# Kernel tuning notes

Hardware: AMD Instinct MI355X
Metric: run time of the kernel (lower is better)

The kernel has to match this reference:

```python
import jax, jax.numpy as jnp
import numpy as np

N = 1048576   # samples
C = 64        # classes (Y unique targets)
S = 8         # subgroups


def setup_inputs() -> dict:
    key = jax.random.key(0)
    k1, k2, k3 = jax.random.split(key, 3)
    logits = jax.random.normal(k1, (N, C), dtype=jnp.float32)
    targets = jax.random.randint(k2, (N,), 0, C, dtype=jnp.int64)
    subgroup_inf = jax.random.randint(k3, (N,), 0, S, dtype=jnp.int64)
    return {"logits": logits, "targets": targets, "subgroup_inf": subgroup_inf}


def reference(logits, targets, subgroup_inf):
    # per-sample cross-entropy (loss_fn with reduction='none')
    logp = jax.nn.log_softmax(logits, axis=-1)                       # [N, C]
    per_sample = -jnp.take_along_axis(logp, targets[:, None], axis=-1)[:, 0]  # [N]

    # composite (target, subgroup) key -> group counts via one scatter-add
    key_ids = targets * S + subgroup_inf                              # [N]
    counts = jax.ops.segment_sum(jnp.ones_like(per_sample), key_ids,
                                 num_segments=C * S)                  # [C*S]
    # every sample's own group has count >= 1, so no div-by-zero
    weighted = per_sample / counts[key_ids]
    return jnp.sum(weighted)
```

## Files before the change

### kernel.cpp

```cpp
#include <hip/hip_runtime.h>


#define NKEYS 512
typedef float v4f __attribute__((ext_vector_type(4)));

__device__ __forceinline__ float pick4(v4f v, int j) {
    float r = v.x;
    r = (j == 1) ? v.y : r;
    r = (j == 2) ? v.z : r;
    r = (j == 3) ? v.w : r;
    return r;
}

__device__ __forceinline__ float esum4(v4f v) {
    return __expf(v.x) + __expf(v.y) + __expf(v.z) + __expf(v.w);
}

__global__ __launch_bounds__(256)
void orl_count_kernel(const int* __restrict__ targets,
                      const int* __restrict__ subg,
                      unsigned int* __restrict__ cnt,
                      int n) {
    __shared__ unsigned int lcnt[NKEYS];
    for (int i = threadIdx.x; i < NKEYS; i += 256) lcnt[i] = 0u;
    __syncthreads();

    const int tid = blockIdx.x * 256 + threadIdx.x;
    const int nthreads = gridDim.x * 256;
    const int n4 = n >> 2;
    for (int i4 = tid; i4 < n4; i4 += nthreads) {
        const int4 t4 = ((const int4*)targets)[i4];
        const int4 u4 = ((const int4*)subg)[i4];
        atomicAdd(&lcnt[t4.x * 8 + u4.x], 1u);
        atomicAdd(&lcnt[t4.y * 8 + u4.y], 1u);
        atomicAdd(&lcnt[t4.z * 8 + u4.z], 1u);
        atomicAdd(&lcnt[t4.w * 8 + u4.w], 1u);
    }
    for (int i = (n4 << 2) + tid; i < n; i += nthreads)
        atomicAdd(&lcnt[targets[i] * 8 + subg[i]], 1u);

    __syncthreads();
    for (int i = threadIdx.x; i < NKEYS; i += 256) {
        const unsigned int c = lcnt[i];
        if (c) atomicAdd(&cnt[i], c);
    }
}

__global__ __launch_bounds__(256, 6)
void orl_main_kernel(const float* __restrict__ logits,
                     const int* __restrict__ targets,
                     const int* __restrict__ subg,
                     const unsigned int* __restrict__ cnt,
                     float* __restrict__ out,
                     int n) {
    __shared__ float lcf[NKEYS];
    for (int i = threadIdx.x; i < NKEYS; i += 256) lcf[i] = (float)cnt[i];
    __syncthreads();

    const int lane = threadIdx.x & 63;
    const int q    = lane & 15;
    const int g    = lane >> 4;
    const int wave = (blockIdx.x << 2) | (threadIdx.x >> 6);
    const int nwaves = gridDim.x << 2;

    float acc = 0.0f;
    int base = wave * 16;
    for (; base + 16 <= n; base += nwaves * 16) {
        const int r0 = base + g * 4;
        const int4 t4 = *(const int4*)(targets + r0);
        const int4 u4 = *(const int4*)(subg + r0);
        const float* rowp = logits + (size_t)r0 * 64 + q * 4;
        const v4f v0 = *(const v4f*)(rowp);
        const v4f v1 = *(const v4f*)(rowp + 64);
        const v4f v2 = *(const v4f*)(rowp + 128);
        const v4f v3 = *(const v4f*)(rowp + 192);

        float s0 = esum4(v0), s1 = esum4(v1), s2 = esum4(v2), s3 = esum4(v3);
        #pragma unroll
        for (int m = 1; m < 16; m <<= 1) {
            s0 += __shfl_xor(s0, m, 16);
            s1 += __shfl_xor(s1, m, 16);
            s2 += __shfl_xor(s2, m, 16);
            s3 += __shfl_xor(s3, m, 16);
        }
        if ((t4.x >> 2) == q)
            acc += (__logf(s0) - pick4(v0, t4.x & 3)) / lcf[t4.x * 8 + u4.x];
        if ((t4.y >> 2) == q)
            acc += (__logf(s1) - pick4(v1, t4.y & 3)) / lcf[t4.y * 8 + u4.y];
        if ((t4.z >> 2) == q)
            acc += (__logf(s2) - pick4(v2, t4.z & 3)) / lcf[t4.z * 8 + u4.z];
        if ((t4.w >> 2) == q)
            acc += (__logf(s3) - pick4(v3, t4.w & 3)) / lcf[t4.w * 8 + u4.w];
    }
    for (int o = 0; o < 4; ++o) {
        const int r = base + g * 4 + o;
        if (r < n) {
            const v4f v = *((const v4f*)(logits + (size_t)r * 64) + q);
            const int t = targets[r];
            float s = esum4(v);
            #pragma unroll
            for (int m = 1; m < 16; m <<= 1) s += __shfl_xor(s, m, 16);
            if ((t >> 2) == q)
                acc += (__logf(s) - pick4(v, t & 3)) / lcf[t * 8 + subg[r]];
        }
    }

    #pragma unroll
    for (int m = 1; m < 64; m <<= 1) acc += __shfl_xor(acc, m, 64);
    __shared__ float wsum[4];
    if (lane == 0) wsum[threadIdx.x >> 6] = acc;
    __syncthreads();
    if (threadIdx.x == 0)
        atomicAdd(out, wsum[0] + wsum[1] + wsum[2] + wsum[3]);
}

extern "C" void kernel_launch(void* const* d_in, const int* in_sizes, int n_in,
                              void* d_out, int out_size, void* d_ws, size_t ws_size,
                              hipStream_t stream) {
    const float* logits  = (const float*)d_in[0];
    const int*   targets = (const int*)d_in[1];
    const int*   subg    = (const int*)d_in[2];
    const int n = in_sizes[1];
    float* out = (float*)d_out;

    unsigned int* cnt = (unsigned int*)d_ws;

    hipMemsetAsync(out, 0, sizeof(float), stream);
    hipMemsetAsync(cnt, 0, NKEYS * sizeof(unsigned int), stream);
    orl_count_kernel<<<256, 256, 0, stream>>>(targets, subg, cnt, n);
    orl_main_kernel<<<2048, 256, 0, stream>>>(logits, targets, subg, cnt, out, n);
}
```

Before: 373.8 us.

## Switch main kernel to one row per thread, drop cross-lane shuffles

Each thread now processes a whole 64-float row: it loads 16 float4 vectors, sums the exponentials locally and reads the target logit directly, replacing the 16-lane-per-row layout that used xor shuffles and predicated selection. The goal is to remove the shuffle reductions and the divergent per-row target handling. The cost is that adjacent threads read addresses 256 bytes apart, so global loads are strided and uncoalesced, and each thread holds more registers. Launch bounds are raised to 8 blocks per CU, and the count kernel grid doubles.

```diff
diff --git a/kernel.cpp b/kernel.cpp
--- a/kernel.cpp
+++ b/kernel.cpp
@@ -3,14 +3,6 @@
 
 #define NKEYS 512
 typedef float v4f __attribute__((ext_vector_type(4)));
-
-__device__ __forceinline__ float pick4(v4f v, int j) {
-    float r = v.x;
-    r = (j == 1) ? v.y : r;
-    r = (j == 2) ? v.z : r;
-    r = (j == 3) ? v.w : r;
-    return r;
-}
 
 __device__ __forceinline__ float esum4(v4f v) {
     return __expf(v.x) + __expf(v.y) + __expf(v.z) + __expf(v.w);
@@ -26,9 +18,9 @@
     __syncthreads();
 
     const int tid = blockIdx.x * 256 + threadIdx.x;
-    const int nthreads = gridDim.x * 256;
+    const int nth = gridDim.x * 256;
     const int n4 = n >> 2;
-    for (int i4 = tid; i4 < n4; i4 += nthreads) {
+    for (int i4 = tid; i4 < n4; i4 += nth) {
         const int4 t4 = ((const int4*)targets)[i4];
         const int4 u4 = ((const int4*)subg)[i4];
         atomicAdd(&lcnt[t4.x * 8 + u4.x], 1u);
@@ -36,7 +28,7 @@
         atomicAdd(&lcnt[t4.z * 8 + u4.z], 1u);
         atomicAdd(&lcnt[t4.w * 8 + u4.w], 1u);
     }
-    for (int i = (n4 << 2) + tid; i < n; i += nthreads)
+    for (int i = (n4 << 2) + tid; i < n; i += nth)
         atomicAdd(&lcnt[targets[i] * 8 + subg[i]], 1u);
 
     __syncthreads();
@@ -46,7 +38,7 @@
     }
 }
 
-__global__ __launch_bounds__(256, 6)
+__global__ __launch_bounds__(256, 8)
 void orl_main_kernel(const float* __restrict__ logits,
                      const int* __restrict__ targets,
                      const int* __restrict__ subg,
@@ -57,58 +49,31 @@
     for (int i = threadIdx.x; i < NKEYS; i += 256) lcf[i] = (float)cnt[i];
     __syncthreads();
 
-    const int lane = threadIdx.x & 63;
-    const int q    = lane & 15;
-    const int g    = lane >> 4;
-    const int wave = (blockIdx.x << 2) | (threadIdx.x >> 6);
-    const int nwaves = gridDim.x << 2;
+    const int tid = blockIdx.x * 256 + threadIdx.x;
+    const int nth = gridDim.x * 256;
 
     float acc = 0.0f;
-    int base = wave * 16;
-    for (; base + 16 <= n; base += nwaves * 16) {
-        const int r0 = base + g * 4;
-        const int4 t4 = *(const int4*)(targets + r0);
-        const int4 u4 = *(const int4*)(subg + r0);
-        const float* rowp = logits + (size_t)r0 * 64 + q * 4;
-        const v4f v0 = *(const v4f*)(rowp);
-        const v4f v1 = *(const v4f*)(rowp + 64);
-        const v4f v2 = *(const v4f*)(rowp + 128);
-        const v4f v3 = *(const v4f*)(rowp + 192);
-
-        float s0 = esum4(v0), s1 = esum4(v1), s2 = esum4(v2), s3 = esum4(v3);
+    for (int r = tid; r < n; r += nth) {
+        const int t = targets[r];
+        const int u = subg[r];
+        const float* rp = logits + (size_t)r * 64;
+        const float xt = rp[t];
+        const v4f* p = (const v4f*)rp;
+        float s = 0.0f;
         #pragma unroll
-        for (int m = 1; m < 16; m <<= 1) {
-            s0 += __shfl_xor(s0, m, 16);
-            s1 += __shfl_xor(s1, m, 16);
-            s2 += __shfl_xor(s2, m, 16);
-            s3 += __shfl_xor(s3, m, 16);
+        for (int h = 0; h < 2; ++h) {
+            const v4f a0 = p[8*h+0], a1 = p[8*h+1], a2 = p[8*h+2], a3 = p[8*h+3];
+            const v4f a4 = p[8*h+4], a5 = p[8*h+5], a6 = p[8*h+6], a7 = p[8*h+7];
+            s += esum4(a0) + esum4(a1) + esum4(a2) + esum4(a3)
+               + esum4(a4) + esum4(a5) + esum4(a6) + esum4(a7);
         }
-        if ((t4.x >> 2) == q)
-            acc += (__logf(s0) - pick4(v0, t4.x & 3)) / lcf[t4.x * 8 + u4.x];
-        if ((t4.y >> 2) == q)
-            acc += (__logf(s1) - pick4(v1, t4.y & 3)) / lcf[t4.y * 8 + u4.y];
-        if ((t4.z >> 2) == q)
-            acc += (__logf(s2) - pick4(v2, t4.z & 3)) / lcf[t4.z * 8 + u4.z];
-        if ((t4.w >> 2) == q)
-            acc += (__logf(s3) - pick4(v3, t4.w & 3)) / lcf[t4.w * 8 + u4.w];
-    }
-    for (int o = 0; o < 4; ++o) {
-        const int r = base + g * 4 + o;
-        if (r < n) {
-            const v4f v = *((const v4f*)(logits + (size_t)r * 64) + q);
-            const int t = targets[r];
-            float s = esum4(v);
-            #pragma unroll
-            for (int m = 1; m < 16; m <<= 1) s += __shfl_xor(s, m, 16);
-            if ((t >> 2) == q)
-                acc += (__logf(s) - pick4(v, t & 3)) / lcf[t * 8 + subg[r]];
-        }
+        acc += (__logf(s) - xt) / lcf[t * 8 + u];
     }
 
     #pragma unroll
     for (int m = 1; m < 64; m <<= 1) acc += __shfl_xor(acc, m, 64);
     __shared__ float wsum[4];
-    if (lane == 0) wsum[threadIdx.x >> 6] = acc;
+    if ((threadIdx.x & 63) == 0) wsum[threadIdx.x >> 6] = acc;
     __syncthreads();
     if (threadIdx.x == 0)
         atomicAdd(out, wsum[0] + wsum[1] + wsum[2] + wsum[3]);
@@ -127,6 +92,6 @@
 
     hipMemsetAsync(out, 0, sizeof(float), stream);
     hipMemsetAsync(cnt, 0, NKEYS * sizeof(unsigned int), stream);
-    orl_count_kernel<<<256, 256, 0, stream>>>(targets, subg, cnt, n);
+    orl_count_kernel<<<512, 256, 0, stream>>>(targets, subg, cnt, n);
     orl_main_kernel<<<2048, 256, 0, stream>>>(logits, targets, subg, cnt, out, n);
 }
```

Measured after the change: 411.6 us. 10.1% more time.

## Accumulate per-key loss sums in LDS and divide by counts once per block

Applied to the files above, without the earlier changes.

The main kernel now adds each per-sample loss into a shared per-key sum with LDS atomics. At the end every block divides each of the 512 key sums by its global count, instead of loading the count and dividing once per sample. Blocks grow to 512 threads with a 512-block grid, logits are read with nontemporal loads, and the count kernel's grid doubles. The trade is float atomics on shared memory in the hot loop, with possible contention, in place of per-sample divisions.

```diff
diff --git a/kernel.cpp b/kernel.cpp
--- a/kernel.cpp
+++ b/kernel.cpp
@@ -2,7 +2,10 @@
 
 
 #define NKEYS 512
+#define ABLOCK 512
 typedef float v4f __attribute__((ext_vector_type(4)));
+
+static_assert(ABLOCK == NKEYS, "flush assumes one key per thread");
 
 __device__ __forceinline__ float pick4(v4f v, int j) {
     float r = v.x;
@@ -26,9 +29,9 @@
     __syncthreads();
 
     const int tid = blockIdx.x * 256 + threadIdx.x;
-    const int nthreads = gridDim.x * 256;
+    const int nth = gridDim.x * 256;
     const int n4 = n >> 2;
-    for (int i4 = tid; i4 < n4; i4 += nthreads) {
+    for (int i4 = tid; i4 < n4; i4 += nth) {
         const int4 t4 = ((const int4*)targets)[i4];
         const int4 u4 = ((const int4*)subg)[i4];
         atomicAdd(&lcnt[t4.x * 8 + u4.x], 1u);
@@ -36,7 +39,7 @@
         atomicAdd(&lcnt[t4.z * 8 + u4.z], 1u);
         atomicAdd(&lcnt[t4.w * 8 + u4.w], 1u);
     }
-    for (int i = (n4 << 2) + tid; i < n; i += nthreads)
+    for (int i = (n4 << 2) + tid; i < n; i += nth)
         atomicAdd(&lcnt[targets[i] * 8 + subg[i]], 1u);
 
     __syncthreads();
@@ -46,34 +49,33 @@
     }
 }
 
-__global__ __launch_bounds__(256, 6)
+__global__ __launch_bounds__(ABLOCK, 4)
 void orl_main_kernel(const float* __restrict__ logits,
                      const int* __restrict__ targets,
                      const int* __restrict__ subg,
                      const unsigned int* __restrict__ cnt,
                      float* __restrict__ out,
                      int n) {
-    __shared__ float lcf[NKEYS];
-    for (int i = threadIdx.x; i < NKEYS; i += 256) lcf[i] = (float)cnt[i];
+    __shared__ float lsum[NKEYS];
+    for (int i = threadIdx.x; i < NKEYS; i += ABLOCK) lsum[i] = 0.0f;
     __syncthreads();
 
     const int lane = threadIdx.x & 63;
     const int q    = lane & 15;
     const int g    = lane >> 4;
-    const int wave = (blockIdx.x << 2) | (threadIdx.x >> 6);
-    const int nwaves = gridDim.x << 2;
+    const int wave = (blockIdx.x << 3) | (threadIdx.x >> 6);
+    const int nwaves = gridDim.x << 3;
 
-    float acc = 0.0f;
     int base = wave * 16;
     for (; base + 16 <= n; base += nwaves * 16) {
         const int r0 = base + g * 4;
         const int4 t4 = *(const int4*)(targets + r0);
         const int4 u4 = *(const int4*)(subg + r0);
         const float* rowp = logits + (size_t)r0 * 64 + q * 4;
-        const v4f v0 = *(const v4f*)(rowp);
-        const v4f v1 = *(const v4f*)(rowp + 64);
-        const v4f v2 = *(const v4f*)(rowp + 128);
-        const v4f v3 = *(const v4f*)(rowp + 192);
+        const v4f v0 = __builtin_nontemporal_load((const v4f*)(rowp));
+        const v4f v1 = __builtin_nontemporal_load((const v4f*)(rowp + 64));
+        const v4f v2 = __builtin_nontemporal_load((const v4f*)(rowp + 128));
+        const v4f v3 = __builtin_nontemporal_load((const v4f*)(rowp + 192));
 
         float s0 = esum4(v0), s1 = esum4(v1), s2 = esum4(v2), s3 = esum4(v3);
         #pragma unroll
@@ -84,13 +86,13 @@
             s3 += __shfl_xor(s3, m, 16);
         }
         if ((t4.x >> 2) == q)
-            acc += (__logf(s0) - pick4(v0, t4.x & 3)) / lcf[t4.x * 8 + u4.x];
+            atomicAdd(&lsum[t4.x * 8 + u4.x], __logf(s0) - pick4(v0, t4.x & 3));
         if ((t4.y >> 2) == q)
-            acc += (__logf(s1) - pick4(v1, t4.y & 3)) / lcf[t4.y * 8 + u4.y];
+            atomicAdd(&lsum[t4.y * 8 + u4.y], __logf(s1) - pick4(v1, t4.y & 3));
         if ((t4.z >> 2) == q)
-            acc += (__logf(s2) - pick4(v2, t4.z & 3)) / lcf[t4.z * 8 + u4.z];
+            atomicAdd(&lsum[t4.z * 8 + u4.z], __logf(s2) - pick4(v2, t4.z & 3));
         if ((t4.w >> 2) == q)
-            acc += (__logf(s3) - pick4(v3, t4.w & 3)) / lcf[t4.w * 8 + u4.w];
+            atomicAdd(&lsum[t4.w * 8 + u4.w], __logf(s3) - pick4(v3, t4.w & 3));
     }
     for (int o = 0; o < 4; ++o) {
         const int r = base + g * 4 + o;
@@ -101,17 +103,27 @@
             #pragma unroll
             for (int m = 1; m < 16; m <<= 1) s += __shfl_xor(s, m, 16);
             if ((t >> 2) == q)
-                acc += (__logf(s) - pick4(v, t & 3)) / lcf[t * 8 + subg[r]];
+                atomicAdd(&lsum[t * 8 + subg[r]], __logf(s) - pick4(v, t & 3));
         }
     }
 
+    __syncthreads();
+    float w = 0.0f;
+    {
+        const unsigned int gc = cnt[threadIdx.x];
+        if (gc) w = lsum[threadIdx.x] / (float)gc;
+    }
     #pragma unroll
-    for (int m = 1; m < 64; m <<= 1) acc += __shfl_xor(acc, m, 64);
-    __shared__ float wsum[4];
-    if (lane == 0) wsum[threadIdx.x >> 6] = acc;
+    for (int m = 1; m < 64; m <<= 1) w += __shfl_xor(w, m, 64);
+    __shared__ float wsum[8];
+    if ((threadIdx.x & 63) == 0) wsum[threadIdx.x >> 6] = w;
     __syncthreads();
-    if (threadIdx.x == 0)
-        atomicAdd(out, wsum[0] + wsum[1] + wsum[2] + wsum[3]);
+    if (threadIdx.x == 0) {
+        float t = 0.0f;
+        #pragma unroll
+        for (int i = 0; i < 8; ++i) t += wsum[i];
+        atomicAdd(out, t);
+    }
 }
 
 extern "C" void kernel_launch(void* const* d_in, const int* in_sizes, int n_in,
@@ -127,6 +139,6 @@
 
     hipMemsetAsync(out, 0, sizeof(float), stream);
     hipMemsetAsync(cnt, 0, NKEYS * sizeof(unsigned int), stream);
-    orl_count_kernel<<<256, 256, 0, stream>>>(targets, subg, cnt, n);
-    orl_main_kernel<<<2048, 256, 0, stream>>>(logits, targets, subg, cnt, out, n);
+    orl_count_kernel<<<512, 256, 0, stream>>>(targets, subg, cnt, n);
+    orl_main_kernel<<<512, ABLOCK, 0, stream>>>(logits, targets, subg, cnt, out, n);
 }
```

After: 356.2 us. 1.05x faster.
